# Performance work log

Hardware: AMD Instinct MI355X
Metric: run time of the kernel (lower is better)

## Reference

```python
import jax, jax.numpy as jnp
import numpy as np

D_MODEL = 1024
NUM_HEADS = 16
D_K = D_MODEL // NUM_HEADS
THETA = 10000.0
BATCH = 2
SEQ = 2048


def apply_rope(x, token_positions):
    # x: [B, H, S, D_K]; token_positions: [S] int
    half = D_K // 2
    inv_freq = THETA ** (-(jnp.arange(half, dtype=jnp.float32) * 2.0) / D_K)  # [half]
    angles = token_positions.astype(jnp.float32)[:, None] * inv_freq[None, :]  # [S, half]
    cos = jnp.cos(angles)  # [S, half]
    sin = jnp.sin(angles)
    x1 = x[..., 0::2]  # even indices
    x2 = x[..., 1::2]  # odd indices
    out_even = x1 * cos - x2 * sin
    out_odd = x1 * sin + x2 * cos
    # interleave back: [..., S, half, 2] -> [..., S, D_K]
    return jnp.stack([out_even, out_odd], axis=-1).reshape(x.shape)


def setup_inputs() -> dict:
    key = jax.random.key(0)
    ks = jax.random.split(key, 5)
    x = jax.random.normal(ks[0], (BATCH, SEQ, D_MODEL), dtype=jnp.float32)
    token_positions = jnp.arange(SEQ, dtype=jnp.int64)
    scale = 0.02
    Wq = jax.random.normal(ks[1], (D_MODEL, D_MODEL), dtype=jnp.float32) * scale
    Wk = jax.random.normal(ks[2], (D_MODEL, D_MODEL), dtype=jnp.float32) * scale
    Wv = jax.random.normal(ks[3], (D_MODEL, D_MODEL), dtype=jnp.float32) * scale
    Wo = jax.random.normal(ks[4], (D_MODEL, D_MODEL), dtype=jnp.float32) * scale
    return {"x": x, "token_positions": token_positions, "Wq": Wq, "Wk": Wk, "Wv": Wv, "Wo": Wo}


def reference(x, token_positions, Wq, Wk, Wv, Wo):
    B, S, _ = x.shape
    # cs336 Linear: y = x @ W.T with W of shape (out, in), no bias
    def proj(W):
        h = jnp.einsum('bsd,od->bso', x, W)
        return h.reshape(B, S, NUM_HEADS, D_K).transpose(0, 2, 1, 3)  # [B,H,S,Dk]
    Q = apply_rope(proj(Wq), token_positions)
    K = apply_rope(proj(Wk), token_positions)
    V = proj(Wv)
    scores = jnp.einsum('bhqd,bhkd->bhqk', Q, K) / jnp.sqrt(jnp.float32(D_K))
    causal = jnp.tril(jnp.ones((S, S), dtype=bool))
    scores = jnp.where(causal, scores, -jnp.inf)
    attn = jax.nn.softmax(scores, axis=-1)
    out = jnp.einsum('bhqk,bhkd->bhqd', attn, V)  # [B,H,S,Dk]
    out = out.transpose(0, 2, 1, 3).reshape(B, S, D_MODEL)
    return jnp.einsum('bsd,od->bso', out, Wo)
```

## Files before the change

### kernel.cpp

```cpp
#include <hip/hip_runtime.h>
#include <hip/hip_bf16.h>
#include <math.h>

#define NHEADS 16
#define DKH 64
#define SEQ 2048
#define DMODEL 1024

typedef __attribute__((ext_vector_type(8))) short short8;
typedef __attribute__((ext_vector_type(4))) float f32x4;

#define GLDS16(g, l)                                         \
  __builtin_amdgcn_global_load_lds(                          \
      (__attribute__((address_space(1))) void*)(void*)(g),   \
      (__attribute__((address_space(3))) void*)(l), 16, 0, 0)

__device__ __forceinline__ short f2bf(float f) {
  unsigned u = __float_as_uint(f);
  unsigned r = (u + 0x7fffu + ((u >> 16) & 1u)) >> 16;
  return (short)r;
}

__device__ __forceinline__ unsigned cvtpk(float lo, float hi) {
  unsigned r;
  asm("v_cvt_pk_bf16_f32 %0, %1, %2" : "=v"(r) : "v"(lo), "v"(hi));
  return r;
}

__device__ __forceinline__ short8 pack8(float4 a, float4 b) {
  short8 v;
  v[0] = f2bf(a.x); v[1] = f2bf(a.y); v[2] = f2bf(a.z); v[3] = f2bf(a.w);
  v[4] = f2bf(b.x); v[5] = f2bf(b.y); v[6] = f2bf(b.z); v[7] = f2bf(b.w);
  return v;
}

__device__ __forceinline__ int swz(int r, int gran) {
  return r * 64 + ((gran ^ (r & 7)) << 3);
}

__global__ __launch_bounds__(256) void precast_rope_kernel(
    const float* __restrict__ X, const float* __restrict__ Wq,
    const float* __restrict__ Wk, const float* __restrict__ Wv,
    const float* __restrict__ Wo, const int* __restrict__ tp,
    short* __restrict__ Xb, short* __restrict__ Wqb, short* __restrict__ Wkb,
    short* __restrict__ Wvb, short* __restrict__ Wob,
    float* __restrict__ ct, float* __restrict__ st) {
  int bid = blockIdx.x;
  if (bid < 4096) {
    int i = bid * 256 + threadIdx.x;
    const float* src; short* dst; int off;
    if (i < 524288) { src = X; dst = Xb; off = i; }
    else {
      int k = i - 524288; int w = k >> 17; off = k & 131071;
      src = (w == 0) ? Wq : (w == 1) ? Wk : (w == 2) ? Wv : Wo;
      dst = (w == 0) ? Wqb : (w == 1) ? Wkb : (w == 2) ? Wvb : Wob;
    }
    const float4* p = reinterpret_cast<const float4*>(src) + 2 * (size_t)off;
    float4 a = p[0], b = p[1];
    reinterpret_cast<short8*>(dst)[off] = pack8(a, b);
  } else {
    int idx = (bid - 4096) * 256 + threadIdx.x;
    if (idx >= SEQ * 32) return;
    int s = idx >> 5, i = idx & 31;
    int is64 = (tp[1] == 0);
    int p = is64 ? tp[2 * s] : tp[s];
    float invf = powf(10000.0f, -(2.0f * (float)i) / 64.0f);
    float a = (float)p * invf;
    ct[idx] = cosf(a);
    st[idx] = sinf(a);
  }
}

__global__ __launch_bounds__(512, 2) void gemm_qkv_kernel(
    const short* __restrict__ X, const short* __restrict__ Wq,
    const short* __restrict__ Wk, const short* __restrict__ Wv,
    short* __restrict__ Qb, short* __restrict__ Kb, short* __restrict__ Vb,
    const float* __restrict__ ct, const float* __restrict__ st) {
  __shared__ __align__(16) short As[2][256 * 64];
  __shared__ __align__(16) short Bs[2][192 * 64];
  const int id = blockIdx.x;
  const int xcd = id & 7, rr = id >> 3;
  const int tm = (xcd & 3) * 4 + (rr & 3);
  const int tn = (xcd >> 2) * 8 + (rr >> 2);
  const int tid = threadIdx.x;
  const int wave = tid >> 6, lane = tid & 63;
  const int l15 = lane & 15, quad = lane >> 4;
  const int wm = wave >> 2, wn = wave & 3;

  const int n0 = tn * 192;
  const short* Abase = X + (size_t)(tm * 256) * DMODEL;
  const short* Bbase = Wq + (size_t)n0 * DMODEL;
  (void)Wk; (void)Wv;

  const int lr = lane >> 3;
  const int lc = (lane & 7) ^ lr;

#define STGA(bufi, half, kt_)                                              \
  do {                                                                     \
    int R0 = (half) * 128 + wave * 16;                                     \
    GLDS16(Abase + (size_t)(R0 + lr) * DMODEL + (kt_) * 64 + lc * 8,       \
           &As[bufi][R0 * 64 + lane * 8]);                                 \
    GLDS16(Abase + (size_t)(R0 + 8 + lr) * DMODEL + (kt_) * 64 + lc * 8,   \
           &As[bufi][(R0 + 8) * 64 + lane * 8]);                           \
  } while (0)
#define STGB(bufi, t, kt_)                                                 \
  do {                                                                     \
    int R0 = (t) * 64 + wave * 8;                                          \
    GLDS16(Bbase + (size_t)(R0 + lr) * DMODEL + (kt_) * 64 + lc * 8,       \
           &Bs[bufi][R0 * 64 + lane * 8]);                                 \
  } while (0)

  f32x4 acc[8][3];
#pragma unroll
  for (int m = 0; m < 8; m++)
#pragma unroll
    for (int n = 0; n < 3; n++) acc[m][n] = (f32x4){0.f, 0.f, 0.f, 0.f};

  STGB(0, 0, 0); STGB(0, 1, 0); STGB(0, 2, 0);
  STGA(0, 0, 0); STGA(0, 1, 0);
  STGB(1, 0, 1); STGB(1, 1, 1); STGB(1, 2, 1);

  short8 bfr[3][2];
  for (int kt = 0; kt < 16; kt++) {
    const int buf = kt & 1;
    if (kt < 15) { STGA(buf ^ 1, 0, kt + 1); }
    if (kt < 15) { asm volatile("s_waitcnt vmcnt(5)" ::: "memory"); }
    else         { asm volatile("s_waitcnt vmcnt(0)" ::: "memory"); }
    asm volatile("s_barrier" ::: "memory");
#pragma unroll
    for (int nb = 0; nb < 3; nb++)
#pragma unroll
      for (int ks = 0; ks < 2; ks++)
        bfr[nb][ks] = *reinterpret_cast<const short8*>(
            &Bs[buf][swz(wn * 48 + nb * 16 + l15, ks * 4 + quad)]);
    {
      short8 af[2][2];
#pragma unroll
      for (int j = 0; j < 2; j++)
#pragma unroll
        for (int ks = 0; ks < 2; ks++)
          af[j][ks] = *reinterpret_cast<const short8*>(
              &As[buf][swz(wm * 128 + j * 16 + l15, ks * 4 + quad)]);
      __builtin_amdgcn_s_setprio(1);
#pragma unroll
      for (int j = 0; j < 2; j++)
#pragma unroll
        for (int nb = 0; nb < 3; nb++)
#pragma unroll
          for (int ks = 0; ks < 2; ks++)
            acc[j][nb] = __builtin_amdgcn_mfma_f32_16x16x32_bf16(
                af[j][ks], bfr[nb][ks], acc[j][nb], 0, 0, 0);
      __builtin_amdgcn_s_setprio(0);
    }
    asm volatile("s_barrier" ::: "memory");
#pragma unroll
    for (int p = 1; p < 4; p++) {
      short8 af[2][2];
#pragma unroll
      for (int j = 0; j < 2; j++)
#pragma unroll
        for (int ks = 0; ks < 2; ks++)
          af[j][ks] = *reinterpret_cast<const short8*>(
              &As[buf][swz(wm * 128 + (p * 2 + j) * 16 + l15, ks * 4 + quad)]);
      if (p == 1)      { if (kt < 15) { STGA(buf ^ 1, 1, kt + 1); } }
      else if (p == 2) { if (kt < 14) { STGB(buf, 0, kt + 2); STGB(buf, 1, kt + 2); } }
      else             { if (kt < 14) { STGB(buf, 2, kt + 2); } }
      asm volatile("s_barrier" ::: "memory");
      __builtin_amdgcn_s_setprio(1);
#pragma unroll
      for (int j = 0; j < 2; j++)
#pragma unroll
        for (int nb = 0; nb < 3; nb++)
#pragma unroll
          for (int ks = 0; ks < 2; ks++)
            acc[p * 2 + j][nb] = __builtin_amdgcn_mfma_f32_16x16x32_bf16(
                af[j][ks], bfr[nb][ks], acc[p * 2 + j][nb], 0, 0, 0);
      __builtin_amdgcn_s_setprio(0);
      asm volatile("s_barrier" ::: "memory");
    }
  }
#undef STGA
#undef STGB

#pragma unroll
  for (int mf = 0; mf < 8; mf++) {
    const int s0g = tm * 256 + wm * 128 + mf * 16 + quad * 4;
    const int b = s0g >> 11, s = s0g & 2047;
#pragma unroll
    for (int nb = 0; nb < 3; nb++) {
      int nl = n0 + wn * 48 + nb * 16 + l15;
      int mid = nl >> 10;
      int c = nl & 1023;
      int h = c >> 6, dd = c & 63;
      if (mid == 2) {
        unsigned u0 = (unsigned)(unsigned short)f2bf(acc[mf][nb][0]) |
                      ((unsigned)(unsigned short)f2bf(acc[mf][nb][1]) << 16);
        unsigned u1 = (unsigned)(unsigned short)f2bf(acc[mf][nb][2]) |
                      ((unsigned)(unsigned short)f2bf(acc[mf][nb][3]) << 16);
        uint2 pk; pk.x = u0; pk.y = u1;
        *reinterpret_cast<uint2*>(Vb + ((size_t)(b * NHEADS + h) * DKH + dd) * SEQ + s) = pk;
      } else {
#pragma unroll
        for (int reg = 0; reg < 4; reg++) {
          float v = acc[mf][nb][reg];
          float pv = __shfl_xor(v, 1);
          int fi = dd >> 1;
          int sg = s + reg;
          float cc = ct[sg * 32 + fi], sn = st[sg * 32 + fi];
          float o = (dd & 1) ? (pv * sn + v * cc) : (v * cc - pv * sn);
          size_t oi = (((size_t)(b * NHEADS + h)) * SEQ + sg) * DKH + dd;
          ((mid == 0) ? Qb : Kb)[oi] = f2bf(o);
        }
      }
    }
  }
}

__global__ __launch_bounds__(256, 4) void attn_kernel(
    const short* __restrict__ Qb, const short* __restrict__ Kb,
    const short* __restrict__ Vtb, short* __restrict__ Ob) {
  __shared__ __align__(16) short QPs[64 * 64];
  __shared__ __align__(16) short Ks[2][64 * 64];
  __shared__ __align__(16) short Vs[2][64 * 64];

  const int id = blockIdx.x;
  const int x8 = id & 7;
  const int c  = (id >> 3) & 31;
  const int q2 = id >> 8;
  const int bh = x8 * 4 + q2;
  const int qt = (q2 == 0) ? c
               : (q2 == 1) ? (31 - c)
               : (q2 == 2) ? ((c + 16) & 31)
               : ((15 - c) & 31);

  const int tid = threadIdx.x;
  const int wave = tid >> 6, lane = tid & 63;
  const int l15 = lane & 15, quad = lane >> 4;
  const int sr0 = tid >> 3, sc = tid & 7;

  const short* Qp = Qb + (size_t)bh * SEQ * DKH;
  const short* Kp = Kb + (size_t)bh * SEQ * DKH;
  const short* Vp = Vtb + (size_t)bh * DKH * SEQ;

  uint4 kreg[2], vreg[2];
#pragma unroll
  for (int i = 0; i < 2; i++) {
    int r = sr0 + i * 32;
    kreg[i] = *reinterpret_cast<const uint4*>(Kp + (size_t)r * DKH + sc * 8);
    vreg[i] = *reinterpret_cast<const uint4*>(Vp + (size_t)r * SEQ + sc * 8);
  }
#pragma unroll
  for (int i = 0; i < 2; i++) {
    int r = sr0 + i * 32;
    uint4 v = *reinterpret_cast<const uint4*>(Qp + (size_t)(qt * 64 + r) * DKH + sc * 8);
    *reinterpret_cast<uint4*>(&QPs[swz(r, sc)]) = v;
  }
#pragma unroll
  for (int i = 0; i < 2; i++) {
    int r = sr0 + i * 32;
    *reinterpret_cast<uint4*>(&Ks[0][swz(r, sc)]) = kreg[i];
    *reinterpret_cast<uint4*>(&Vs[0][swz(r, sc)]) = vreg[i];
  }
  __syncthreads();
  short8 qf0, qf1;
  {
    int r = wave * 16 + l15;
    qf0 = *reinterpret_cast<const short8*>(&QPs[swz(r, quad)]);
    qf1 = *reinterpret_cast<const short8*>(&QPs[swz(r, 4 + quad)]);
  }
  __syncthreads();

  f32x4 accO[4];
#pragma unroll
  for (int i = 0; i < 4; i++) accO[i] = (f32x4){0.f, 0.f, 0.f, 0.f};
  float rs = 0.f;

  const float SCL = 0.125f * 1.44269504089f;
  const float FM = 13.0f;

  int buf = 0;
  for (int kt = 0; kt <= qt; kt++) {
    if (kt < qt) {
#pragma unroll
      for (int i = 0; i < 2; i++) {
        int r = sr0 + i * 32;
        kreg[i] = *reinterpret_cast<const uint4*>(Kp + (size_t)((kt + 1) * 64 + r) * DKH + sc * 8);
        vreg[i] = *reinterpret_cast<const uint4*>(Vp + (size_t)r * SEQ + (kt + 1) * 64 + sc * 8);
      }
    }

    f32x4 sa[4];
    __builtin_amdgcn_s_setprio(1);
#pragma unroll
    for (int nb = 0; nb < 4; nb++) {
      sa[nb] = (f32x4){0.f, 0.f, 0.f, 0.f};
      int r = nb * 16 + l15;
      short8 kf0 = *reinterpret_cast<const short8*>(&Ks[buf][swz(r, quad)]);
      sa[nb] = __builtin_amdgcn_mfma_f32_16x16x32_bf16(kf0, qf0, sa[nb], 0, 0, 0);
      short8 kf1 = *reinterpret_cast<const short8*>(&Ks[buf][swz(r, 4 + quad)]);
      sa[nb] = __builtin_amdgcn_mfma_f32_16x16x32_bf16(kf1, qf1, sa[nb], 0, 0, 0);
    }
    __builtin_amdgcn_s_setprio(0);

    const bool diag = (kt == qt);
    const int prow = wave * 16 + l15;
#pragma unroll
    for (int nb = 0; nb < 4; nb++) {
      float p0 = exp2f(sa[nb][0] * SCL - FM);
      float p1 = exp2f(sa[nb][1] * SCL - FM);
      float p2 = exp2f(sa[nb][2] * SCL - FM);
      float p3 = exp2f(sa[nb][3] * SCL - FM);
      if (diag) {
        int kbase = nb * 16 + quad * 4;
        if (kbase + 0 > prow) p0 = 0.f;
        if (kbase + 1 > prow) p1 = 0.f;
        if (kbase + 2 > prow) p2 = 0.f;
        if (kbase + 3 > prow) p3 = 0.f;
      }
      rs += (p0 + p1) + (p2 + p3);
      uint2 pk; pk.x = cvtpk(p0, p1); pk.y = cvtpk(p2, p3);
      int g2 = 2 * nb + (quad >> 1);
      *reinterpret_cast<uint2*>(&QPs[swz(prow, g2) + (quad & 1) * 4]) = pk;
    }

    short8 pf0 = *reinterpret_cast<const short8*>(&QPs[swz(prow, quad)]);
    short8 pf1 = *reinterpret_cast<const short8*>(&QPs[swz(prow, 4 + quad)]);
    __builtin_amdgcn_s_setprio(1);
#pragma unroll
    for (int db = 0; db < 4; db++) {
      int dv = db * 16 + l15;
      short8 vf0 = *reinterpret_cast<const short8*>(&Vs[buf][swz(dv, quad)]);
      accO[db] = __builtin_amdgcn_mfma_f32_16x16x32_bf16(pf0, vf0, accO[db], 0, 0, 0);
      short8 vf1 = *reinterpret_cast<const short8*>(&Vs[buf][swz(dv, 4 + quad)]);
      accO[db] = __builtin_amdgcn_mfma_f32_16x16x32_bf16(pf1, vf1, accO[db], 0, 0, 0);
    }
    __builtin_amdgcn_s_setprio(0);

    if (kt < qt) {
      int nbuf = buf ^ 1;
#pragma unroll
      for (int i = 0; i < 2; i++) {
        int r = sr0 + i * 32;
        *reinterpret_cast<uint4*>(&Ks[nbuf][swz(r, sc)]) = kreg[i];
        *reinterpret_cast<uint4*>(&Vs[nbuf][swz(r, sc)]) = vreg[i];
      }
      __syncthreads();
      buf = nbuf;
    }
  }

  float t = rs;
  t += __shfl_xor(t, 16);
  t += __shfl_xor(t, 32);
  float lv[4];
#pragma unroll
  for (int reg = 0; reg < 4; reg++) lv[reg] = __shfl(t, quad * 4 + reg);

  int b = bh >> 4, h = bh & 15;
#pragma unroll
  for (int db = 0; db < 4; db++)
#pragma unroll
    for (int reg = 0; reg < 4; reg++) {
      int s = qt * 64 + wave * 16 + quad * 4 + reg;
      int dv = db * 16 + l15;
      float o = accO[db][reg] / lv[reg];
      Ob[((size_t)(b * SEQ + s)) * DMODEL + h * DKH + dv] = f2bf(o);
    }
}

__global__ __launch_bounds__(256) void gemm_out_kernel(
    const short* __restrict__ X, const short* __restrict__ Wo, float* __restrict__ Out) {
  __shared__ __align__(16) short As[128 * 64];
  __shared__ __align__(16) short Bs[64 * 64];
  const int tm = blockIdx.x;
  const int tn = blockIdx.y;
  const int tid = threadIdx.x;
  const int wave = tid >> 6, lane = tid & 63;
  const int l15 = lane & 15, quad = lane >> 4;
  const int wm = wave >> 1, wn = wave & 1;

  const short* Abase = X + (size_t)(tm * 128) * DMODEL;
  const short* Bbase = Wo + (size_t)(tn * 64) * DMODEL;

  const int lr = lane >> 3;
  const int lc = (lane & 7) ^ lr;

  f32x4 acc[4][2];
#pragma unroll
  for (int mb = 0; mb < 4; mb++)
#pragma unroll
    for (int nb = 0; nb < 2; nb++) acc[mb][nb] = (f32x4){0.f, 0.f, 0.f, 0.f};

  for (int kk = 0; kk < 16; kk++) {
    const short* Ak = Abase + kk * 64;
    const short* Bk = Bbase + kk * 64;
#pragma unroll
    for (int i = 0; i < 4; i++) {
      int R = i * 32 + wave * 8;
      GLDS16(Ak + (size_t)(R + lr) * DMODEL + lc * 8, &As[R * 64 + lane * 8]);
    }
#pragma unroll
    for (int i = 0; i < 2; i++) {
      int R = i * 32 + wave * 8;
      GLDS16(Bk + (size_t)(R + lr) * DMODEL + lc * 8, &Bs[R * 64 + lane * 8]);
    }
    __syncthreads();
#pragma unroll
    for (int kg = 0; kg < 2; kg++) {
      short8 af[4], bf[2];
#pragma unroll
      for (int mb = 0; mb < 4; mb++) {
        int r = wm * 64 + mb * 16 + l15;
        af[mb] = *reinterpret_cast<const short8*>(&As[swz(r, kg * 4 + quad)]);
      }
#pragma unroll
      for (int nb = 0; nb < 2; nb++) {
        int r = wn * 32 + nb * 16 + l15;
        bf[nb] = *reinterpret_cast<const short8*>(&Bs[swz(r, kg * 4 + quad)]);
      }
#pragma unroll
      for (int mb = 0; mb < 4; mb++)
#pragma unroll
        for (int nb = 0; nb < 2; nb++)
          acc[mb][nb] = __builtin_amdgcn_mfma_f32_16x16x32_bf16(af[mb], bf[nb], acc[mb][nb], 0, 0, 0);
    }
    __syncthreads();
  }
#pragma unroll
  for (int mb = 0; mb < 4; mb++)
#pragma unroll
    for (int nb = 0; nb < 2; nb++)
#pragma unroll
      for (int reg = 0; reg < 4; reg++) {
        int rg = tm * 128 + wm * 64 + mb * 16 + quad * 4 + reg;
        int col = tn * 64 + wn * 32 + nb * 16 + l15;
        Out[(size_t)rg * DMODEL + col] = acc[mb][nb][reg];
      }
}

extern "C" void kernel_launch(void* const* d_in, const int* in_sizes, int n_in,
                              void* d_out, int out_size, void* d_ws, size_t ws_size,
                              hipStream_t stream) {
  (void)in_sizes; (void)n_in; (void)out_size; (void)ws_size;
  const float* X  = (const float*)d_in[0];
  const int*   tp = (const int*)d_in[1];
  const float* Wq = (const float*)d_in[2];
  const float* Wk = (const float*)d_in[3];
  const float* Wv = (const float*)d_in[4];
  const float* Wo = (const float*)d_in[5];
  float* Out = (float*)d_out;

  short* Qb  = (short*)d_ws;
  short* Kb  = Qb + 4194304;
  short* Vb  = Kb + 4194304;
  short* Ab  = Vb + 4194304;
  short* Xb  = Ab + 4194304;
  short* Wqb = Xb + 4194304;
  short* Wkb = Wqb + 1048576;
  short* Wvb = Wkb + 1048576;
  short* Wob = Wvb + 1048576;
  float* ct  = (float*)(Wob + 1048576);
  float* st  = ct + SEQ * 32;

  precast_rope_kernel<<<dim3(4352), dim3(256), 0, stream>>>(
      X, Wq, Wk, Wv, Wo, tp, Xb, Wqb, Wkb, Wvb, Wob, ct, st);
  gemm_qkv_kernel<<<dim3(256), dim3(512), 0, stream>>>(Xb, Wqb, Wkb, Wvb,
                                                       Qb, Kb, Vb, ct, st);
  attn_kernel<<<dim3(1024), dim3(256), 0, stream>>>(Qb, Kb, Vb, Ab);
  gemm_out_kernel<<<dim3(32, 16), dim3(256), 0, stream>>>(Ab, Wob, Out);
}
```

Measured before the change: 185.9 us.

## Keep P in registers and permute V reads to match MFMA layout

Drops the shared-memory staging buffer for Q and P. Q fragments now load straight from global into registers. The softmax probabilities are packed directly into MFMA A-operand registers, and the V fragment reads are permuted (two 8-byte LDS reads per half) so the k-index ordering matches the register-resident P layout. This removes an LDS write/read round trip per tile and one barrier, and frees 8KB of LDS. In exchange, V reads become narrower 64-bit accesses.

```diff
diff --git a/kernel.cpp b/kernel.cpp
--- a/kernel.cpp
+++ b/kernel.cpp
@@ -219,7 +219,6 @@
 __global__ __launch_bounds__(256, 4) void attn_kernel(
     const short* __restrict__ Qb, const short* __restrict__ Kb,
     const short* __restrict__ Vtb, short* __restrict__ Ob) {
-  __shared__ __align__(16) short QPs[64 * 64];
   __shared__ __align__(16) short Ks[2][64 * 64];
   __shared__ __align__(16) short Vs[2][64 * 64];
 
@@ -249,24 +248,17 @@
     kreg[i] = *reinterpret_cast<const uint4*>(Kp + (size_t)r * DKH + sc * 8);
     vreg[i] = *reinterpret_cast<const uint4*>(Vp + (size_t)r * SEQ + sc * 8);
   }
-#pragma unroll
-  for (int i = 0; i < 2; i++) {
-    int r = sr0 + i * 32;
-    uint4 v = *reinterpret_cast<const uint4*>(Qp + (size_t)(qt * 64 + r) * DKH + sc * 8);
-    *reinterpret_cast<uint4*>(&QPs[swz(r, sc)]) = v;
+  short8 qf0, qf1;
+  {
+    const short* qrow = Qp + (size_t)(qt * 64 + wave * 16 + l15) * DKH;
+    qf0 = *reinterpret_cast<const short8*>(qrow + quad * 8);
+    qf1 = *reinterpret_cast<const short8*>(qrow + (4 + quad) * 8);
   }
 #pragma unroll
   for (int i = 0; i < 2; i++) {
     int r = sr0 + i * 32;
     *reinterpret_cast<uint4*>(&Ks[0][swz(r, sc)]) = kreg[i];
     *reinterpret_cast<uint4*>(&Vs[0][swz(r, sc)]) = vreg[i];
-  }
-  __syncthreads();
-  short8 qf0, qf1;
-  {
-    int r = wave * 16 + l15;
-    qf0 = *reinterpret_cast<const short8*>(&QPs[swz(r, quad)]);
-    qf1 = *reinterpret_cast<const short8*>(&QPs[swz(r, 4 + quad)]);
   }
   __syncthreads();
 
@@ -304,6 +296,7 @@
 
     const bool diag = (kt == qt);
     const int prow = wave * 16 + l15;
+    unsigned pu[4], pw[4];
 #pragma unroll
     for (int nb = 0; nb < 4; nb++) {
       float p0 = exp2f(sa[nb][0] * SCL - FM);
@@ -318,20 +311,32 @@
         if (kbase + 3 > prow) p3 = 0.f;
       }
       rs += (p0 + p1) + (p2 + p3);
-      uint2 pk; pk.x = cvtpk(p0, p1); pk.y = cvtpk(p2, p3);
-      int g2 = 2 * nb + (quad >> 1);
-      *reinterpret_cast<uint2*>(&QPs[swz(prow, g2) + (quad & 1) * 4]) = pk;
-    }
-
-    short8 pf0 = *reinterpret_cast<const short8*>(&QPs[swz(prow, quad)]);
-    short8 pf1 = *reinterpret_cast<const short8*>(&QPs[swz(prow, 4 + quad)]);
+      pu[nb] = cvtpk(p0, p1);
+      pw[nb] = cvtpk(p2, p3);
+    }
+
+    short8 pf0, pf1;
+    {
+      unsigned* w0 = reinterpret_cast<unsigned*>(&pf0);
+      w0[0] = pu[0]; w0[1] = pw[0]; w0[2] = pu[1]; w0[3] = pw[1];
+      unsigned* w1 = reinterpret_cast<unsigned*>(&pf1);
+      w1[0] = pu[2]; w1[1] = pw[2]; w1[2] = pu[3]; w1[3] = pw[3];
+    }
+    const int qh = quad >> 1, qo = (quad & 1) * 4;
     __builtin_amdgcn_s_setprio(1);
 #pragma unroll
     for (int db = 0; db < 4; db++) {
       int dv = db * 16 + l15;
-      short8 vf0 = *reinterpret_cast<const short8*>(&Vs[buf][swz(dv, quad)]);
+      short8 vf0, vf1;
+      {
+        uint2* v0 = reinterpret_cast<uint2*>(&vf0);
+        v0[0] = *reinterpret_cast<const uint2*>(&Vs[buf][swz(dv, qh) + qo]);
+        v0[1] = *reinterpret_cast<const uint2*>(&Vs[buf][swz(dv, 2 + qh) + qo]);
+        uint2* v1 = reinterpret_cast<uint2*>(&vf1);
+        v1[0] = *reinterpret_cast<const uint2*>(&Vs[buf][swz(dv, 4 + qh) + qo]);
+        v1[1] = *reinterpret_cast<const uint2*>(&Vs[buf][swz(dv, 6 + qh) + qo]);
+      }
       accO[db] = __builtin_amdgcn_mfma_f32_16x16x32_bf16(pf0, vf0, accO[db], 0, 0, 0);
-      short8 vf1 = *reinterpret_cast<const short8*>(&Vs[buf][swz(dv, 4 + quad)]);
       accO[db] = __builtin_amdgcn_mfma_f32_16x16x32_bf16(pf1, vf1, accO[db], 0, 0, 0);
     }
     __builtin_amdgcn_s_setprio(0);
```

After: 185.9 us. About the same (-0.0%).
